# Kernel optimization log

Measured on AMD Instinct MI355X. Metric: run time of the kernel, lower is better.

Reference implementation:

```python
import jax, jax.numpy as jnp
import numpy as np

# SLAYER neuron / simulation hyperparameters (from network.yaml)
THETA = 10.0      # spike threshold
TAU_SR = 10.0     # SRM (PSP) kernel time constant [ms]
TAU_REF = 1.0     # refractory kernel time constant [ms]
SCALE_REF = 2.0   # refractory kernel scale
TS = 1.0          # simulation step [ms]
K_SRM = 100       # truncation length of SRM kernel (eps decays ~0 by 10*tau)
K_REF = 32        # truncation length of refractory kernel (tauRef=1 -> decays fast)


def _eps_kernel(tau, k):
    # eps(t) = (t/tau) * exp(1 - t/tau), eps(0) = 0  (SLAYER SRM alpha kernel)
    t = jnp.arange(k, dtype=jnp.float32) * TS
    return (t / tau) * jnp.exp(1.0 - t / tau)


def psp(x, kern):
    # Causal temporal filter: y[..., t] = sum_j kern[j] * x[..., t - j]
    B, N, T = x.shape
    lhs = x.reshape(B * N, 1, T)
    rhs = kern[::-1].reshape(1, 1, -1)  # lax.conv is cross-correlation -> flip
    y = jax.lax.conv_general_dilated(
        lhs, rhs, window_strides=(1,), padding=[(kern.shape[0] - 1, 0)],
        dimension_numbers=('NCH', 'OIH', 'NCH'))
    return y.reshape(B, N, T)


def spike(u, refk):
    # Sequential thresholding with refractory feedback (SLAYER spikeFunction fwd).
    # u: [B, N, T] membrane drive. State r: future refractory contributions.
    kr = refk.shape[0]
    refk_shift = jnp.concatenate([refk[1:], jnp.zeros((1,), refk.dtype)])

    def step(r, u_t):
        m = u_t + r[..., 0]                      # membrane potential at t
        s = (m >= THETA).astype(u_t.dtype)       # hard spike
        r_next = jnp.concatenate([r[..., 1:], jnp.zeros_like(r[..., :1])], -1) \
                 + s[..., None] * refk_shift     # add refractory response
        return r_next, s

    uT = jnp.moveaxis(u, -1, 0)                  # [T, B, N]
    r0 = jnp.zeros(uT.shape[1:] + (kr,), u.dtype)
    _, sT = jax.lax.scan(step, r0, uT)
    return jnp.moveaxis(sT, 0, -1) / TS          # [B, N, T]


def setup_inputs() -> dict:
    key = jax.random.key(0)
    k1, k2, k3 = jax.random.split(key, 3)
    B, NIN, NHID, NOUT, T = 32, 2048, 512, 10, 350
    spike_input = (jax.random.uniform(k1, (B, NIN, T)) < 0.05).astype(jnp.float32)
    W1 = jax.random.normal(k2, (NHID, NIN), dtype=jnp.float32) * 0.05
    W2 = jax.random.normal(k3, (NOUT, NHID), dtype=jnp.float32) * 0.05
    return {"spike_input": spike_input, "W1": W1, "W2": W2}


def reference(spike_input, W1, W2):
    srm = _eps_kernel(TAU_SR, K_SRM)
    refk = -SCALE_REF * THETA * _eps_kernel(TAU_REF, K_REF)
    # layer 1: psp -> dense -> spike
    a1 = jnp.einsum('bnt,mn->bmt', psp(spike_input, srm), W1)
    s1 = spike(a1, refk)
    # layer 2: psp -> dense -> spike
    a2 = jnp.einsum('bnt,mn->bmt', psp(s1, srm), W2)
    s2 = spike(a2, refk)
    return s2
```

## Files before the change

### kernel.cpp

```cpp
#include <hip/hip_runtime.h>
#include <stdint.h>

static constexpr int B  = 32;
static constexpr int T  = 350;
static constexpr int NIN = 2048;
static constexpr int NH  = 512;
static constexpr int NO  = 10;
static constexpr int BT  = B * T;

static constexpr float THETA = 10.0f;
static constexpr float BETA  = 0.36787944117144233f;
static constexpr float CREF  = 54.365636569180904707f;

static constexpr size_t OFF_W1TS = 0;
static constexpr size_t OFF_MASK = 4196352;
static constexpr size_t OFF_SRM  = 7080960;
static constexpr size_t OFF_Z1   = 7081984;
static constexpr size_t OFF_A1   = 30019584;
static constexpr size_t OFF_LST  = OFF_A1;
static constexpr size_t OFF_CNT  = OFF_A1 + 4300800;
static constexpr size_t OFF_SMK  = 52957184;

static constexpr int SLICE_F = 8;
static constexpr int NSLICE  = NH / SLICE_F;
static constexpr int SLICE_STRIDE = 2049 * SLICE_F;

__global__ void __launch_bounds__(256) k_prep(const float* __restrict__ x,
                                              const float* __restrict__ W1,
                                              float* __restrict__ W1Ts,
                                              uint64_t* __restrict__ mask,
                                              float* __restrict__ srm28) {
    int bid = blockIdx.x;
    if (bid < 1024) {
        __shared__ uint64_t tb[6][64];
        int b = bid >> 5, nblk = bid & 31;
        int wv = threadIdx.x >> 6, lane = threadIdx.x & 63;
        for (int g = 0; g < 4; ++g) {
            float v[4][6];
            #pragma unroll
            for (int i = 0; i < 4; ++i) {
                int nr = wv + 4 * (4 * g + i);
                const float* xp = x + ((size_t)b * NIN + nblk * 64 + nr) * T;
                #pragma unroll
                for (int c = 0; c < 6; ++c) {
                    int t = c * 64 + lane;
                    v[i][c] = (t < T) ? xp[t] : 0.f;
                }
            }
            #pragma unroll
            for (int i = 0; i < 4; ++i) {
                int nr = wv + 4 * (4 * g + i);
                #pragma unroll
                for (int c = 0; c < 6; ++c) {
                    uint64_t mk = __ballot(v[i][c] != 0.0f);
                    if (lane == 0) tb[c][nr] = mk;
                }
            }
        }
        __syncthreads();
        static const uint64_t AM[6] = {
            0x00000000FFFFFFFFull, 0x0000FFFF0000FFFFull, 0x00FF00FF00FF00FFull,
            0x0F0F0F0F0F0F0F0Full, 0x3333333333333333ull, 0x5555555555555555ull };
        for (int c = wv; c < 6; c += 4) {
            uint64_t w = tb[c][lane];
            #pragma unroll
            for (int i = 0; i < 6; ++i) {
                int s = 32 >> i;
                uint64_t A = AM[i];
                uint64_t y = __shfl_xor((unsigned long long)w, s);
                if ((lane & s) == 0) w = (w & A)  | ((y & A) << s);
                else                 w = (w & ~A) | ((y & ~A) >> s);
            }
            int t = c * 64 + lane;
            if (t < T) mask[((size_t)b * 32 + nblk) * 352 + t] = w;
        }
    } else if (bid < 2048) {
        __shared__ float tile[32][33];
        int idx = bid - 1024;
        int n0 = (idx & 63) * 32, m0 = (idx >> 6) * 32;
        int tx = threadIdx.x & 31, ty0 = threadIdx.x >> 5;
        #pragma unroll
        for (int i = 0; i < 4; ++i) {
            int ty = ty0 + 8 * i;
            tile[ty][tx] = W1[(size_t)(m0 + ty) * NIN + n0 + tx];
        }
        __syncthreads();
        #pragma unroll
        for (int i = 0; i < 4; ++i) {
            int ty = ty0 + 8 * i;
            int n = n0 + ty, m = m0 + tx;
            W1Ts[(size_t)(m >> 3) * SLICE_STRIDE + n * SLICE_F + (m & 7)] = tile[tx][ty];
        }
    } else {
        int j = threadIdx.x;
        if (j < 192) {
            float v = 0.f;
            int i = j - 28;
            if (i >= 0 && i < 100) { float t = (float)i; v = (t * 0.1f) * expf(1.f - t * 0.1f); }
            srm28[j] = v;
        }
        for (int i = j; i < NSLICE * SLICE_F; i += 256)
            W1Ts[(size_t)(i >> 3) * SLICE_STRIDE + 2048 * SLICE_F + (i & 7)] = 0.f;
    }
}

__global__ void __launch_bounds__(64) k_decode(const uint64_t* __restrict__ mask,
                                               uint16_t* __restrict__ glst,
                                               int* __restrict__ gcnt) {
    __shared__ uint16_t lst[192];
    int t = blockIdx.x, b = blockIdx.y;
    int row = b * T + t;
    int lane = threadIdx.x;
    uint64_t w = (lane < 32) ? mask[((size_t)b * 32 + lane) * 352 + t] : 0ull;
    int cnt = __popcll(w);
    int pre = cnt;
    #pragma unroll
    for (int off = 1; off < 64; off <<= 1) {
        int v = __shfl_up(pre, off);
        if (lane >= off) pre += v;
    }
    int total = __shfl(pre, 63);
    int excl = pre - cnt;
    while (w) {
        int bit = __builtin_ctzll(w);
        w &= w - 1;
        lst[excl++] = (uint16_t)((lane << 6) + bit);
    }
    int padded = (total + 7) & ~7;
    if (lane < padded - total) lst[total + lane] = 2048;
    __syncthreads();
    uint16_t* op = glst + (size_t)row * 192;
    for (int i = lane; i < padded; i += 64) op[i] = lst[i];
    if (lane == 0) gcnt[row] = padded;
}

__global__ void __launch_bounds__(256) k_z1s(const uint16_t* __restrict__ glst,
                                             const int* __restrict__ gcnt,
                                             const float* __restrict__ W1Ts,
                                             float* __restrict__ z1) {
    __shared__ float w1s[SLICE_STRIDE];
    int s = blockIdx.x;
    int bt0 = blockIdx.y * (BT / 8);
    const float4* src = (const float4*)(W1Ts + (size_t)s * SLICE_STRIDE);
    for (int i = threadIdx.x; i < SLICE_STRIDE / 4; i += 256)
        ((float4*)w1s)[i] = src[i];
    __syncthreads();

    int q  = threadIdx.x & 1;
    int rl = threadIdx.x >> 1;
    for (int rr = rl; rr < BT / 8; rr += 128) {
        int row = bt0 + rr;
        int padded = gcnt[row];
        const ushort4* lp = (const ushort4*)(glst + (size_t)row * 192);
        float4 acc = {0, 0, 0, 0};
        for (int k = 0; k < padded; k += 8) {
            ushort4 q0 = lp[k >> 2];
            ushort4 q1 = lp[(k >> 2) + 1];
            const float* base = w1s + q * 4;
            float4 x0 = *(const float4*)(base + q0.x * SLICE_F);
            float4 x1 = *(const float4*)(base + q0.y * SLICE_F);
            float4 x2 = *(const float4*)(base + q0.z * SLICE_F);
            float4 x3 = *(const float4*)(base + q0.w * SLICE_F);
            float4 x4 = *(const float4*)(base + q1.x * SLICE_F);
            float4 x5 = *(const float4*)(base + q1.y * SLICE_F);
            float4 x6 = *(const float4*)(base + q1.z * SLICE_F);
            float4 x7 = *(const float4*)(base + q1.w * SLICE_F);
            acc.x += x0.x; acc.y += x0.y; acc.z += x0.z; acc.w += x0.w;
            acc.x += x1.x; acc.y += x1.y; acc.z += x1.z; acc.w += x1.w;
            acc.x += x2.x; acc.y += x2.y; acc.z += x2.z; acc.w += x2.w;
            acc.x += x3.x; acc.y += x3.y; acc.z += x3.z; acc.w += x3.w;
            acc.x += x4.x; acc.y += x4.y; acc.z += x4.z; acc.w += x4.w;
            acc.x += x5.x; acc.y += x5.y; acc.z += x5.z; acc.w += x5.w;
            acc.x += x6.x; acc.y += x6.y; acc.z += x6.z; acc.w += x6.w;
            acc.x += x7.x; acc.y += x7.y; acc.z += x7.z; acc.w += x7.w;
        }
        *(float4*)(z1 + (size_t)row * NH + s * SLICE_F + q * 4) = acc;
    }
}

__global__ void __launch_bounds__(64) k_fir1(const float* __restrict__ src,
                                             float* __restrict__ dst,
                                             const float* __restrict__ srm28) {
    __shared__ float tb[192];
    int b = blockIdx.x, half = blockIdx.y, tg = blockIdx.z;
    int lane = threadIdx.x;
    for (int i = lane; i < 192; i += 64) tb[i] = srm28[i];
    __syncthreads();
    int t0 = tg * 16;
    int m = half * 256 + lane * 4;
    const float* sp = src + (size_t)b * T * NH + m;

    float4 acc[16];
    #pragma unroll
    for (int r = 0; r < 16; ++r) acc[r] = make_float4(0.f, 0.f, 0.f, 0.f);
    float c[16];
    #pragma unroll
    for (int r = 0; r < 16; ++r) c[r] = tb[r + 127];

    for (int o = 0; o < 8; ++o) {
        #pragma unroll
        for (int j = 0; j < 16; ++j) {
            int dd = o * 16 + j;
            int tau = t0 - 99 + dd;
            float4 v = make_float4(0.f, 0.f, 0.f, 0.f);
            if (tau >= 0 && tau < T) v = *(const float4*)(sp + (size_t)tau * NH);
            #pragma unroll
            for (int r = 0; r < 16; ++r) {
                acc[r].x += c[r] * v.x; acc[r].y += c[r] * v.y;
                acc[r].z += c[r] * v.z; acc[r].w += c[r] * v.w;
            }
            #pragma unroll
            for (int r = 15; r > 0; --r) c[r] = c[r - 1];
            int ci = 126 - dd;
            c[0] = tb[ci < 0 ? 0 : ci];
        }
    }
    #pragma unroll
    for (int r = 0; r < 16; ++r) {
        int t = t0 + r;
        if (t < T) *(float4*)(dst + ((size_t)b * T + t) * NH + m) = acc[r];
    }
}

__global__ void __launch_bounds__(64) k_scan1(const float* __restrict__ a1,
                                              uint64_t* __restrict__ smaskg) {
    constexpr int CT = 16;
    constexpr int NC = (T + CT - 1) / CT;
    int tid = blockIdx.x * 64 + threadIdx.x;
    int b = tid >> 9, m = tid & 511;
    int w8 = m >> 6;
    const float* up = a1 + (size_t)b * T * NH + m;
    float A = 0.f, Bs = 0.f;
    float c0[CT], c1[CT], c2[CT];
    #pragma unroll
    for (int j = 0; j < CT; ++j) c0[j] = up[(size_t)j * NH];
    #pragma unroll
    for (int j = 0; j < CT; ++j) {
        int t = CT + j;
        c1[j] = (t < T) ? up[(size_t)t * NH] : 0.f;
    }
    for (int c = 0; c < NC; ++c) {
        int t0 = c * CT;
        int nsteps = (T - t0 < CT) ? (T - t0) : CT;
        if (c + 2 < NC) {
            #pragma unroll
            for (int j = 0; j < CT; ++j) {
                int t = t0 + 2 * CT + j;
                c2[j] = (t < T) ? up[(size_t)t * NH] : 0.f;
            }
        }
        #pragma unroll
        for (int j = 0; j < CT; ++j) {
            if (j < nsteps) {
                float mem = c0[j] - CREF * Bs;
                float sp = (mem >= THETA) ? 1.0f : 0.0f;
                A = sp + BETA * A;
                Bs = BETA * (Bs + A);
                uint64_t mk = __ballot(sp != 0.0f);
                if (threadIdx.x == 0) smaskg[((size_t)b * T + t0 + j) * 8 + w8] = mk;
            }
        }
        #pragma unroll
        for (int j = 0; j < CT; ++j) { c0[j] = c1[j]; c1[j] = c2[j]; }
    }
}

__global__ void __launch_bounds__(256) k_tail(const uint64_t* __restrict__ smaskg,
                                              const float* __restrict__ W2,
                                              const float* __restrict__ srm28,
                                              float* __restrict__ out) {
    __shared__ float w2s_ab[NO * NH];
    __shared__ uint64_t smk[T * 8];
    __shared__ float tb[192];
    __shared__ float zb[350 * 11 + 16];
    int b = blockIdx.x, tid = threadIdx.x;
    for (int i = tid; i < NO * NH; i += 256) w2s_ab[i] = W2[i];
    const uint64_t* mp = smaskg + (size_t)b * T * 8;
    for (int i = tid; i < T * 8; i += 256) smk[i] = mp[i];
    if (tid < 192) tb[tid] = srm28[tid];
    __syncthreads();
    for (int i = tid; i < T * NO; i += 256) {
        int t = i / NO, o = i - t * NO;
        const float* wrow = w2s_ab + o * NH;
        float acc = 0.f;
        #pragma unroll
        for (int w8 = 0; w8 < 8; ++w8) {
            uint64_t mk = smk[t * 8 + w8];
            int base = w8 * 64;
            while (mk) {
                int bit = __builtin_ctzll(mk);
                mk &= mk - 1;
                acc += wrow[base + bit];
            }
        }
        zb[t * 11 + o] = acc;
    }
    __syncthreads();
    float* ab = w2s_ab;
    if (tid < 220) {
        int tt = tid / 10, o = tid - tt * 10;
        int t0 = tt * 16;
        float acc[16];
        #pragma unroll
        for (int r = 0; r < 16; ++r) acc[r] = 0.f;
        float c[16];
        #pragma unroll
        for (int r = 0; r < 16; ++r) c[r] = tb[r + 127];
        for (int oo = 0; oo < 8; ++oo) {
            #pragma unroll
            for (int j = 0; j < 16; ++j) {
                int dd = oo * 16 + j;
                int tau = t0 - 99 + dd;
                float v = (tau >= 0 && tau < T) ? zb[tau * 11 + o] : 0.f;
                #pragma unroll
                for (int r = 0; r < 16; ++r) acc[r] += c[r] * v;
                #pragma unroll
                for (int r = 15; r > 0; --r) c[r] = c[r - 1];
                int ci = 126 - dd;
                c[0] = tb[ci < 0 ? 0 : ci];
            }
        }
        #pragma unroll
        for (int r = 0; r < 16; ++r) {
            int t = t0 + r;
            if (t < T) ab[t * 10 + o] = acc[r];
        }
    }
    __syncthreads();
    if (tid < NO) {
        int o = tid;
        float A2 = 0.f, B2 = 0.f;
        float* op = out + ((size_t)b * NO + o) * T;
        for (int t = 0; t < T; ++t) {
            float mem = ab[t * 10 + o] - CREF * B2;
            float sp = (mem >= THETA) ? 1.0f : 0.0f;
            A2 = sp + BETA * A2;
            B2 = BETA * (B2 + A2);
            op[t] = sp;
        }
    }
}

extern "C" void kernel_launch(void* const* d_in, const int* in_sizes, int n_in,
                              void* d_out, int out_size, void* d_ws, size_t ws_size,
                              hipStream_t stream) {
    const float* x  = (const float*)d_in[0];
    const float* W1 = (const float*)d_in[1];
    const float* W2 = (const float*)d_in[2];
    char* ws = (char*)d_ws;
    float*    W1Ts   = (float*)(ws + OFF_W1TS);
    uint64_t* mask   = (uint64_t*)(ws + OFF_MASK);
    float*    srm    = (float*)(ws + OFF_SRM);
    float*    z1     = (float*)(ws + OFF_Z1);
    float*    a1     = (float*)(ws + OFF_A1);
    uint16_t* glst   = (uint16_t*)(ws + OFF_LST);
    int*      gcnt   = (int*)(ws + OFF_CNT);
    uint64_t* smaskg = (uint64_t*)(ws + OFF_SMK);
    float*    out    = (float*)d_out;

    hipLaunchKernelGGL(k_prep,   dim3(2049),      dim3(256), 0, stream, x, W1, W1Ts, mask, srm);
    hipLaunchKernelGGL(k_decode, dim3(T, B),      dim3(64),  0, stream, mask, glst, gcnt);
    hipLaunchKernelGGL(k_z1s,    dim3(NSLICE, 8), dim3(256), 0, stream, glst, gcnt, W1Ts, z1);
    hipLaunchKernelGGL(k_fir1,   dim3(B, 2, 22),  dim3(64),  0, stream, z1, a1, srm);
    hipLaunchKernelGGL(k_scan1,  dim3(256),       dim3(64),  0, stream, a1, smaskg);
    hipLaunchKernelGGL(k_tail,   dim3(B),         dim3(256), 0, stream, smaskg, W2, srm, out);
}
```

Measured before the change: 297.8 us.

## Skip zero-history FIR blocks with windowed coefficients and split z1 launch

The FIR kernel for layer 1 now starts its outer loop at the first block that can hold valid time indices. It loads a 31-entry coefficient window per block instead of shifting a 16-register coefficient array on every step. The two-tap tail is handled separately, and the padded zero block is dropped. Separately, the sparse z1 gather kernel is launched as two half-grids over weight slices, which adds a launch and may change scheduling; it risks more register pressure from the 31-entry window.

```diff
diff --git a/kernel.cpp b/kernel.cpp
--- a/kernel.cpp
+++ b/kernel.cpp
@@ -137,9 +137,10 @@
 __global__ void __launch_bounds__(256) k_z1s(const uint16_t* __restrict__ glst,
                                              const int* __restrict__ gcnt,
                                              const float* __restrict__ W1Ts,
-                                             float* __restrict__ z1) {
+                                             float* __restrict__ z1,
+                                             int soff) {
     __shared__ float w1s[SLICE_STRIDE];
-    int s = blockIdx.x;
+    int s = blockIdx.x + soff;
     int bt0 = blockIdx.y * (BT / 8);
     const float4* src = (const float4*)(W1Ts + (size_t)s * SLICE_STRIDE);
     for (int i = threadIdx.x; i < SLICE_STRIDE / 4; i += 256)
@@ -193,26 +194,44 @@
     float4 acc[16];
     #pragma unroll
     for (int r = 0; r < 16; ++r) acc[r] = make_float4(0.f, 0.f, 0.f, 0.f);
-    float c[16];
-    #pragma unroll
-    for (int r = 0; r < 16; ++r) c[r] = tb[r + 127];
-
-    for (int o = 0; o < 8; ++o) {
+
+    int o_start = (99 - t0) >> 4;
+    if (o_start < 0) o_start = 0;
+
+    for (int o = o_start; o < 7; ++o) {
+        float cw[31];
+        int cb = 112 - 16 * o;
+        #pragma unroll
+        for (int k = 0; k < 31; ++k) cw[k] = tb[cb + k];
+        int dd0 = o * 16;
         #pragma unroll
         for (int j = 0; j < 16; ++j) {
-            int dd = o * 16 + j;
-            int tau = t0 - 99 + dd;
+            int tau = t0 - 99 + dd0 + j;
             float4 v = make_float4(0.f, 0.f, 0.f, 0.f);
             if (tau >= 0 && tau < T) v = *(const float4*)(sp + (size_t)tau * NH);
             #pragma unroll
             for (int r = 0; r < 16; ++r) {
-                acc[r].x += c[r] * v.x; acc[r].y += c[r] * v.y;
-                acc[r].z += c[r] * v.z; acc[r].w += c[r] * v.w;
-            }
-            #pragma unroll
-            for (int r = 15; r > 0; --r) c[r] = c[r - 1];
-            int ci = 126 - dd;
-            c[0] = tb[ci < 0 ? 0 : ci];
+                float c = cw[r - j + 15];
+                acc[r].x += c * v.x; acc[r].y += c * v.y;
+                acc[r].z += c * v.z; acc[r].w += c * v.w;
+            }
+        }
+    }
+    {
+        float e1 = tb[29], e2 = tb[30];
+        int tau = t0 + 13;
+        if (tau < T) {
+            float4 v = *(const float4*)(sp + (size_t)tau * NH);
+            acc[14].x += e1 * v.x; acc[14].y += e1 * v.y;
+            acc[14].z += e1 * v.z; acc[14].w += e1 * v.w;
+            acc[15].x += e2 * v.x; acc[15].y += e2 * v.y;
+            acc[15].z += e2 * v.z; acc[15].w += e2 * v.w;
+        }
+        tau = t0 + 14;
+        if (tau < T) {
+            float4 v = *(const float4*)(sp + (size_t)tau * NH);
+            acc[15].x += e1 * v.x; acc[15].y += e1 * v.y;
+            acc[15].z += e1 * v.z; acc[15].w += e1 * v.w;
         }
     }
     #pragma unroll
@@ -358,10 +377,11 @@
     uint64_t* smaskg = (uint64_t*)(ws + OFF_SMK);
     float*    out    = (float*)d_out;
 
-    hipLaunchKernelGGL(k_prep,   dim3(2049),      dim3(256), 0, stream, x, W1, W1Ts, mask, srm);
-    hipLaunchKernelGGL(k_decode, dim3(T, B),      dim3(64),  0, stream, mask, glst, gcnt);
-    hipLaunchKernelGGL(k_z1s,    dim3(NSLICE, 8), dim3(256), 0, stream, glst, gcnt, W1Ts, z1);
-    hipLaunchKernelGGL(k_fir1,   dim3(B, 2, 22),  dim3(64),  0, stream, z1, a1, srm);
-    hipLaunchKernelGGL(k_scan1,  dim3(256),       dim3(64),  0, stream, a1, smaskg);
-    hipLaunchKernelGGL(k_tail,   dim3(B),         dim3(256), 0, stream, smaskg, W2, srm, out);
-}
+    hipLaunchKernelGGL(k_prep,   dim3(2049),          dim3(256), 0, stream, x, W1, W1Ts, mask, srm);
+    hipLaunchKernelGGL(k_decode, dim3(T, B),          dim3(64),  0, stream, mask, glst, gcnt);
+    hipLaunchKernelGGL(k_z1s,    dim3(NSLICE/2, 8),   dim3(256), 0, stream, glst, gcnt, W1Ts, z1, 0);
+    hipLaunchKernelGGL(k_z1s,    dim3(NSLICE/2, 8),   dim3(256), 0, stream, glst, gcnt, W1Ts, z1, NSLICE/2);
+    hipLaunchKernelGGL(k_fir1,   dim3(B, 2, 22),      dim3(64),  0, stream, z1, a1, srm);
+    hipLaunchKernelGGL(k_scan1,  dim3(256),           dim3(64),  0, stream, a1, smaskg);
+    hipLaunchKernelGGL(k_tail,   dim3(B),             dim3(256), 0, stream, smaskg, W2, srm, out);
+}
```

After: 321.4 us. +7.9%, slower.
